# Optimization experiments

Measured on AMD Instinct MI355X. Metric: run time of the kernel, lower is better.

## Reference

```python
import jax, jax.numpy as jnp
import numpy as np

B, L, G, N, K, E = 64, 512, 128, 32, 8, 65536
NTOK, D_TOK, H_DIR, NTL_INP, NHID, NREL = 10000, 64, 64, 32, 16, 16


def _bn(x, gamma, beta, eps=1e-5):
    # training-mode BatchNorm1d over axis 0; x: (n, C)
    mu = x.mean(0)
    var = x.var(0)
    return gamma * (x - mu) / jnp.sqrt(var + eps) + beta


def _lstm(x, w_ih, w_hh, b_ih, b_hh):
    # x: (B, T, D); torch gate order i, f, g, o
    nb = x.shape[0]
    H = w_hh.shape[1]
    def step(carry, xt):
        h, c = carry
        g = xt @ w_ih.T + b_ih + h @ w_hh.T + b_hh
        i, f, gg, o = jnp.split(g, 4, axis=-1)
        c = jax.nn.sigmoid(f) * c + jax.nn.sigmoid(i) * jnp.tanh(gg)
        h = jax.nn.sigmoid(o) * jnp.tanh(c)
        return (h, c), h
    init = (jnp.zeros((nb, H), x.dtype), jnp.zeros((nb, H), x.dtype))
    _, hs = jax.lax.scan(step, init, jnp.swapaxes(x, 0, 1))
    return jnp.swapaxes(hs, 0, 1)


def setup_inputs() -> dict:
    key = jax.random.key(0)
    ks = jax.random.split(key, 24)
    inp = {}
    inp['seq'] = jax.random.randint(ks[0], (B, L), 0, NTOK)
    inp['pos2grp'] = jax.random.randint(ks[1], (B, L), 0, G)
    inp['idx'] = jax.random.randint(ks[2], (B, N, K), 0, L)
    inp['u'] = jax.random.randint(ks[3], (E,), 0, B * N)
    inp['v'] = jax.random.randint(ks[4], (E,), 0, B * N)
    # parameters
    s = 1.0 / np.sqrt(H_DIR)
    inp['tok_emb'] = jax.random.normal(ks[5], (NTOK, D_TOK), jnp.float32)
    for tag, k0 in (('f', 6), ('b', 10)):
        inp[f'w_ih_{tag}'] = s * jax.random.normal(ks[k0], (4 * H_DIR, D_TOK), jnp.float32)
        inp[f'w_hh_{tag}'] = s * jax.random.normal(ks[k0 + 1], (4 * H_DIR, H_DIR), jnp.float32)
        inp[f'b_ih_{tag}'] = s * jax.random.normal(ks[k0 + 2], (4 * H_DIR,), jnp.float32)
        inp[f'b_hh_{tag}'] = s * jax.random.normal(ks[k0 + 3], (4 * H_DIR,), jnp.float32)
    inp['w_src'] = (1.0 / np.sqrt(2 * H_DIR)) * jax.random.normal(ks[14], (NTL_INP, 2 * H_DIR), jnp.float32)
    inp['b_src'] = jnp.zeros((NTL_INP,), jnp.float32)
    inp['w_dst'] = (1.0 / np.sqrt(2 * H_DIR)) * jax.random.normal(ks[15], (NTL_INP, 2 * H_DIR), jnp.float32)
    inp['b_dst'] = jnp.zeros((NTL_INP,), jnp.float32)
    inp['g_src'] = jnp.ones((NTL_INP,), jnp.float32)
    inp['be_src'] = jnp.zeros((NTL_INP,), jnp.float32)
    inp['g_dst'] = jnp.ones((NTL_INP,), jnp.float32)
    inp['be_dst'] = jnp.zeros((NTL_INP,), jnp.float32)
    inp['ntl_w'] = 0.001 * jax.random.normal(ks[16], (NREL, NHID, NTL_INP, NTL_INP), jnp.float32)
    inp['ntl_v'] = 0.001 * jax.random.normal(ks[17], (NREL, NHID, 2 * NTL_INP), jnp.float32)
    inp['ntl_b'] = jnp.zeros((NREL, NHID, 1), jnp.float32)
    inp['ntl_u'] = 0.001 * jax.random.normal(ks[18], (NREL, 1, NHID), jnp.float32)
    inp['ntl_g'] = jnp.ones((NREL * NHID,), jnp.float32)
    inp['ntl_be'] = jnp.zeros((NREL * NHID,), jnp.float32)
    return inp


def reference(seq, pos2grp, idx, u, v, tok_emb,
              w_ih_f, w_hh_f, b_ih_f, b_hh_f,
              w_ih_b, w_hh_b, b_ih_b, b_hh_b,
              w_src, b_src, w_dst, b_dst,
              g_src, be_src, g_dst, be_dst,
              ntl_w, ntl_v, ntl_b, ntl_u, ntl_g, ntl_be):
    # token embed + scatter-sum tokens -> groups
    x_tok = tok_emb[seq]                                   # (B, L, D)
    gid = (pos2grp + jnp.arange(B)[:, None] * G).reshape(-1)
    x_grp = jax.ops.segment_sum(x_tok.reshape(B * L, -1), gid,
                                num_segments=B * G).reshape(B, G, -1)
    # bidirectional LSTM over groups
    hf = _lstm(x_grp, w_ih_f, w_hh_f, b_ih_f, b_hh_f)
    hb = jnp.flip(_lstm(jnp.flip(x_grp, 1), w_ih_b, w_hh_b, b_ih_b, b_hh_b), 1)
    h_grp = jnp.concatenate([hf, hb], -1)                  # (B, G, 2H)
    # hierarchical gather + sum: node <- sum over K token positions' groups
    b_idx = jnp.arange(B)[:, None, None]
    g_idx = pos2grp[b_idx, idx]                            # (B, N, K)
    h = h_grp[b_idx, g_idx].sum(2).reshape(B * N, -1)      # (B*N, 2H)
    # edge endpoint projections + batchnorm
    hs = _bn(h[u] @ w_src.T + b_src, g_src, be_src)        # (E, ninp)
    ht = _bn(h[v] @ w_dst.T + b_dst, g_dst, be_dst)
    # Neural Tensor Layer
    linear = jnp.einsum('rhd,nd->rhn', ntl_v, jnp.concatenate([hs, ht], 1))
    bil = jnp.stack([
        jnp.einsum('nhj,nj->hn', jnp.einsum('ni,hij->nhj', hs, ntl_w[r]), ht)
        for r in range(NREL)], 0)                          # (R, H, E)
    z = bil + linear + ntl_b
    mu = z.mean(-1, keepdims=True)
    var = z.var(-1, keepdims=True)
    zn = ntl_g.reshape(NREL, NHID, 1) * (z - mu) / jnp.sqrt(var + 1e-5) \
         + ntl_be.reshape(NREL, NHID, 1)
    t = jnp.tanh(zn)
    logit = jnp.einsum('rh,rhn->nr', ntl_u[:, 0, :], t)    # (E, R)
    return logit
```

## Files before the change

kernel.cpp:

```cpp
#include <hip/hip_runtime.h>
#include <hip/hip_bf16.h>
#include <hip/hip_fp16.h>
#include <cstdint>

constexpr int B_   = 64;
constexpr int L_   = 512;
constexpr int G_   = 128;
constexpr int E_   = 65536;
constexpr int RH   = 256;
constexpr int M_   = 2048;
constexpr int JA   = 33;
constexpr int COLS = RH * JA;

typedef _Float16 v2h __attribute__((ext_vector_type(2)));

#define DEV static __device__ __forceinline__

DEV float sigm(float x) { return 1.f / (1.f + __expf(-x)); }
DEV float tanh_fast(float x) {
    x = fminf(15.f, fmaxf(-15.f, x));
    float e = __expf(2.f * x);
    return (e - 1.f) / (e + 1.f);
}
DEV int rfl(int x) { return __builtin_amdgcn_readfirstlane(x); }
DEV v2h bch(unsigned int x) { union { unsigned int u; v2h h; } c; c.u = x; return c.h; }

__global__ __launch_bounds__(256) void k_waug(const float* __restrict__ ntlw,
                                              const float* __restrict__ ntlv,
                                              const float* __restrict__ ntlb,
                                              float* __restrict__ waug) {
    int gid = blockIdx.x * 256 + threadIdx.x;
    int i   = gid / COLS;
    int rem = gid - i * COLS;
    int j   = rem >> 8;
    int rh  = rem & 255;
    float val;
    if (i < 32) val = (j < 32) ? ntlw[((size_t)rh * 32 + i) * 32 + j] : ntlv[rh * 64 + i];
    else        val = (j < 32) ? ntlv[rh * 64 + 32 + j] : ntlb[rh];
    waug[gid] = val;
}

__global__ __launch_bounds__(256) void k_eh(const int* __restrict__ seq,
                                            const int* __restrict__ p2g,
                                            const float* __restrict__ emb,
                                            const int* __restrict__ u,
                                            const int* __restrict__ v,
                                            float* __restrict__ xg,
                                            int* __restrict__ cu, int* __restrict__ cv) {
    int blk = blockIdx.x;
    int t   = threadIdx.x;
    if (blk >= 64) {
        int n = (blk - 64) * 256 + t;
        atomicAdd(&cu[u[n]], 1);
        atomicAdd(&cv[v[n]], 1);
        return;
    }
    __shared__ float xgl[G_ * 64];
    for (int i = t; i < G_ * 64; i += 256) xgl[i] = 0.f;
    __syncthreads();
    int b = blk;
    int d = t & 63, part = t >> 6;
#pragma unroll 8
    for (int l = part; l < L_; l += 4) {
        int s = seq[b * L_ + l];
        int g = p2g[b * L_ + l];
        atomicAdd(&xgl[g * 64 + d], emb[s * 64 + d]);
    }
    __syncthreads();
    for (int i = t; i < G_ * 64; i += 256) xg[(size_t)b * G_ * 64 + i] = xgl[i];
}

__global__ __launch_bounds__(256) void k_pre(const float* __restrict__ xg,
                                             const float* __restrict__ wihf,
                                             const float* __restrict__ bihf,
                                             const float* __restrict__ bhhf,
                                             const float* __restrict__ wihb,
                                             const float* __restrict__ bihb,
                                             const float* __restrict__ bhhb,
                                             float* __restrict__ pre,
                                             const int* __restrict__ cu,
                                             int* __restrict__ ustart,
                                             int* __restrict__ ucursor) {
    int blk = blockIdx.x;
    int t   = threadIdx.x;
    if (blk == 512) {
        __shared__ int ps[256];
        int base = t * 8, run = 0;
        int c[8], loc[8];
#pragma unroll
        for (int i = 0; i < 8; i++) c[i] = cu[base + i];
#pragma unroll
        for (int i = 0; i < 8; i++) { loc[i] = run; run += c[i]; }
        ps[t] = run;
        __syncthreads();
        for (int off = 1; off < 256; off <<= 1) {
            int a = (t >= off) ? ps[t - off] : 0;
            __syncthreads();
            ps[t] += a;
            __syncthreads();
        }
        int ex = ps[t] - run;
#pragma unroll
        for (int i = 0; i < 8; i++) { ustart[base + i] = ex + loc[i]; ucursor[base + i] = ex + loc[i]; }
        if (t == 255) ustart[2048] = E_;
        return;
    }
    int dir = blk >> 8;
    const float* wih = dir ? wihb : wihf;
    float bias = dir ? (bihb[t] + bhhb[t]) : (bihf[t] + bhhf[t]);
    int r0 = (blk & 255) * 32;

    float4 wv[16];
#pragma unroll
    for (int c = 0; c < 16; c++) wv[c] = ((const float4*)(wih + t * 64))[c];

#pragma unroll 2
    for (int ml = 0; ml < 32; ml++) {
        const float* xr = xg + (size_t)(r0 + ml) * 64;
        float acc = bias;
#pragma unroll
        for (int c = 0; c < 16; c++) {
            float x0 = xr[4 * c], x1 = xr[4 * c + 1], x2 = xr[4 * c + 2], x3 = xr[4 * c + 3];
            acc += x0 * wv[c].x + x1 * wv[c].y + x2 * wv[c].z + x3 * wv[c].w;
        }
        pre[((size_t)dir * 8192 + r0 + ml) * 256 + t] = acc;
    }
}

template <int HALF>
__global__ __launch_bounds__(256, 1) void k_lstm_h(const float* __restrict__ pre,
                                                   const float* __restrict__ whh_f,
                                                   const float* __restrict__ whh_b,
                                                   float* __restrict__ hgrp,
                                                   float* __restrict__ hstate,
                                                   float* __restrict__ cstate,
                                                   const int* __restrict__ u,
                                                   const int* __restrict__ v,
                                                   int* __restrict__ ucursor,
                                                   int2* __restrict__ eonv) {
    int blk = blockIdx.x;
    int t   = threadIdx.x;
    if (HALF == 0 && blk >= 128) {
        int n = (blk - 128) * 256 + t;
        int pos = atomicAdd(&ucursor[u[n]], 1);
        eonv[pos] = make_int2(n, v[n]);
        return;
    }
    __shared__ __align__(16) float plds[64][256];
    __shared__ __align__(16) float hist[64][64];
    __shared__ float gl[2][256];
    int dir = blk >> 6;
    int b   = blk & 63;
    const float* whh = dir ? whh_b : whh_f;
    const float* src = pre + ((size_t)dir * 8192 + (size_t)b * G_) * 256;
    int e = t & 63;
    int q = t >> 6;

    float4 wv[16];
#pragma unroll
    for (int c = 0; c < 16; c++) wv[c] = ((const float4*)(whh + (size_t)t * 64))[c];

    float h, creg;
    if (HALF == 0) { h = 0.f; creg = 0.f; }
    else           { h = hstate[blk * 64 + e]; creg = cstate[blk * 64 + e]; }

    {
        int base = (dir ^ HALF) ? 64 : 0;
        const float4* s4 = (const float4*)(src + (size_t)base * 256);
        float4* d4 = (float4*)&plds[0][0];
#pragma unroll
        for (int i = 0; i < 16; i++) d4[i * 256 + t] = s4[i * 256 + t];
    }
    __syncthreads();
    for (int kk = 0; kk < 64; kk++) {
        int srow = dir ? (63 - kk) : kk;
        float p = plds[srow][t];
        float a0 = p, a1 = 0.f, a2 = 0.f, a3 = 0.f;
#pragma unroll
        for (int c = 0; c < 16; c++) {
            float f0 = __int_as_float(__builtin_amdgcn_readlane(__float_as_int(h), 4 * c + 0));
            float f1 = __int_as_float(__builtin_amdgcn_readlane(__float_as_int(h), 4 * c + 1));
            float f2 = __int_as_float(__builtin_amdgcn_readlane(__float_as_int(h), 4 * c + 2));
            float f3 = __int_as_float(__builtin_amdgcn_readlane(__float_as_int(h), 4 * c + 3));
            a0 += wv[c].x * f0;
            a1 += wv[c].y * f1;
            a2 += wv[c].z * f2;
            a3 += wv[c].w * f3;
        }
        float g = (a0 + a1) + (a2 + a3);
        gl[kk & 1][t] = (q == 2) ? tanh_fast(g) : sigm(g);
        __syncthreads();
        float ai = gl[kk & 1][e];
        float af = gl[kk & 1][64 + e];
        float ag = gl[kk & 1][128 + e];
        float ao = gl[kk & 1][192 + e];
        creg = af * creg + ai * ag;
        h = ao * tanh_fast(creg);
        if (q == 0) hist[srow][e] = h;
    }
    __syncthreads();
    int sbase = (dir ? (1 - HALF) : HALF) * 64;
#pragma unroll
    for (int i = 0; i < 16; i++) {
        int row = q * 16 + i;
        int s = sbase + row;
        hgrp[((size_t)(b * G_ + s)) * 128 + dir * 64 + e] = hist[row][e];
    }
    if (HALF == 0 && q == 0) {
        hstate[blk * 64 + e] = h;
        cstate[blk * 64 + e] = creg;
    }
}

__global__ __launch_bounds__(256) void k_gp(const int* __restrict__ idx,
                                            const int* __restrict__ p2g,
                                            const float* __restrict__ hgrp,
                                            const int* __restrict__ cu,
                                            const int* __restrict__ cv,
                                            const float* __restrict__ wsrc,
                                            const float* __restrict__ bsrc,
                                            const float* __restrict__ wdst,
                                            const float* __restrict__ bdst,
                                            float* __restrict__ Ps, float* __restrict__ Pd,
                                            float* __restrict__ bn_raw) {
    __shared__ __align__(16) float hsl[8][128];
    __shared__ float red[256];
    int m0 = blockIdx.x * 8;
    int t  = threadIdx.x;
    int d = t & 127, mh = t >> 7;
#pragma unroll
    for (int rep = 0; rep < 4; rep++) {
        int ml = rep * 2 + mh;
        int m  = m0 + ml;
        int b  = m >> 5;
        float acc = 0.f;
#pragma unroll
        for (int k = 0; k < 8; k++) {
            int l = idx[m * 8 + k];
            int g = p2g[b * L_ + l];
            acc += hgrp[((size_t)b * G_ + g) * 128 + d];
        }
        hsl[ml][d] = acc;
    }
    __syncthreads();
    int ml = t >> 5, o = t & 31;
    int m  = m0 + ml;
    const float4* hp = (const float4*)&hsl[ml][0];
    float cw_u = (float)cu[m], cw_v = (float)cv[m];
#pragma unroll 1
    for (int side = 0; side < 2; side++) {
        const float* W = side ? wdst : wsrc;
        float4 wr[32];
#pragma unroll
        for (int c = 0; c < 32; c++) wr[c] = ((const float4*)(W + (size_t)o * 128))[c];
        float acc = side ? bdst[o] : bsrc[o];
#pragma unroll
        for (int c = 0; c < 32; c++) {
            float4 h4 = hp[c];
            acc += h4.x * wr[c].x + h4.y * wr[c].y + h4.z * wr[c].z + h4.w * wr[c].w;
        }
        (side ? Pd : Ps)[(size_t)m * 32 + o] = acc;
        float cw = side ? cw_v : cw_u;
        red[t] = cw * acc;
        __syncthreads();
        if (t < 32) {
            float s = 0.f;
#pragma unroll
            for (int i = 0; i < 8; i++) s += red[i * 32 + t];
            atomicAdd(&bn_raw[side * 64 + t], s);
        }
        __syncthreads();
        red[t] = cw * acc * acc;
        __syncthreads();
        if (t < 32) {
            float s = 0.f;
#pragma unroll
            for (int i = 0; i < 8; i++) s += red[i * 32 + t];
            atomicAdd(&bn_raw[side * 64 + 32 + t], s);
        }
        __syncthreads();
    }
}

__global__ __launch_bounds__(256) void k_prep(const float* __restrict__ Ps,
                                              const float* __restrict__ Pd,
                                              const float* __restrict__ bn_raw,
                                              const float* __restrict__ gs,
                                              const float* __restrict__ bes,
                                              const float* __restrict__ gd,
                                              const float* __restrict__ bed,
                                              float* __restrict__ hsaugT,
                                              v2h* __restrict__ htp) {
    int blk = blockIdx.x;
    int t   = threadIdx.x;
    constexpr float invE = 1.f / (float)E_;
    if (blk < 264) {
        int gid = blk * 256 + t;
        int c = gid >> 11;
        int m = gid & 2047;
        float val = 1.f;
        if (c < 32) {
            float mu  = bn_raw[c] * invE;
            float isd = rsqrtf(bn_raw[32 + c] * invE - mu * mu + 1e-5f);
            val = gs[c] * (Ps[(size_t)m * 32 + c] - mu) * isd + bes[c];
        }
        hsaugT[(size_t)c * 2048 + m] = val;
        return;
    }
    int gid = (blk - 264) * 256 + t;
    int m  = gid >> 4;
    int jp = gid & 15;
    int j0 = 2 * jp, j1 = 2 * jp + 1;
    float mu0  = bn_raw[64 + j0] * invE;
    float isd0 = rsqrtf(bn_raw[96 + j0] * invE - mu0 * mu0 + 1e-5f);
    float mu1  = bn_raw[64 + j1] * invE;
    float isd1 = rsqrtf(bn_raw[96 + j1] * invE - mu1 * mu1 + 1e-5f);
    float h0 = gd[j0] * (Pd[(size_t)m * 32 + j0] - mu0) * isd0 + bed[j0];
    float h1 = gd[j1] * (Pd[(size_t)m * 32 + j1] - mu1) * isd1 + bed[j1];
    v2h p;
    p.x = (_Float16)h0; p.y = (_Float16)h1;
    htp[gid] = p;
}

__global__ __launch_bounds__(256) void k_agemm(const float* __restrict__ hsaugT,
                                               const float* __restrict__ waug,
                                               v2h* __restrict__ Ah,
                                               float* __restrict__ A32) {
    int mt = blockIdx.x;
    int jp = blockIdx.y;
    int t  = threadIdx.x;
    if (jp < 16) {
        float w0[JA], w1[JA];
#pragma unroll
        for (int i = 0; i < JA; i++) {
            w0[i] = waug[(size_t)i * COLS + (2 * jp) * 256 + t];
            w1[i] = waug[(size_t)i * COLS + (2 * jp + 1) * 256 + t];
        }
        float acc0[32], acc1[32];
#pragma unroll
        for (int ml = 0; ml < 32; ml++) { acc0[ml] = 0.f; acc1[ml] = 0.f; }
#pragma unroll 3
        for (int i = 0; i < JA; i++) {
            const float* hr = hsaugT + (size_t)i * 2048 + mt * 32;
#pragma unroll
            for (int ml = 0; ml < 32; ml++) {
                acc0[ml] += hr[ml] * w0[i];
                acc1[ml] += hr[ml] * w1[i];
            }
        }
#pragma unroll
        for (int ml = 0; ml < 32; ml++) {
            v2h p;
            p.x = (_Float16)acc0[ml]; p.y = (_Float16)acc1[ml];
            Ah[(size_t)(mt * 32 + ml) * 4096 + jp * 256 + t] = p;
        }
    } else {
        float w2[JA];
#pragma unroll
        for (int i = 0; i < JA; i++) w2[i] = waug[(size_t)i * COLS + 32 * 256 + t];
        float acc[32];
#pragma unroll
        for (int ml = 0; ml < 32; ml++) acc[ml] = 0.f;
#pragma unroll 3
        for (int i = 0; i < JA; i++) {
            const float* hr = hsaugT + (size_t)i * 2048 + mt * 32;
#pragma unroll
            for (int ml = 0; ml < 32; ml++) acc[ml] += hr[ml] * w2[i];
        }
#pragma unroll
        for (int ml = 0; ml < 32; ml++)
            A32[(size_t)(mt * 32 + ml) * 256 + t] = acc[ml];
    }
}

DEV void load_htp(unsigned int* d, const unsigned int* __restrict__ htp, int vv) {
    const unsigned int* hp = htp + vv * 16;
#pragma unroll
    for (int i = 0; i < 16; i++) d[i] = hp[i];
}
DEV void edge_fd(const unsigned int* av, const unsigned int* ht, float av32,
                 int n, int t, _Float16* __restrict__ zh, float& s1, float& s2) {
    float acc = av32;
#pragma unroll
    for (int jp = 0; jp < 16; jp++)
        acc = __builtin_amdgcn_fdot2(bch(av[jp]), bch(ht[jp]), acc, false);
    zh[(size_t)n * 256 + t] = (_Float16)acc;
    s1 += acc; s2 += acc * acc;
}

__global__ __launch_bounds__(256) void k_z(const unsigned int* __restrict__ Ah,
                                           const float* __restrict__ A32,
                                           const unsigned int* __restrict__ htp,
                                           const int* __restrict__ ustart,
                                           const int2* __restrict__ eonv,
                                           _Float16* __restrict__ zh,
                                           float* __restrict__ zsum,
                                           float* __restrict__ zsq) {
    int t  = threadIdx.x;
    int uu = blockIdx.x;
    float s1 = 0.f, s2 = 0.f;
    unsigned int av[16];
#pragma unroll
    for (int jp = 0; jp < 16; jp++)
        av[jp] = Ah[(size_t)uu * 4096 + jp * 256 + t];
    float av32 = A32[(size_t)uu * 256 + t];
    int e0 = ustart[uu], e1 = ustart[uu + 1];
    if (e0 < e1) {
        int e = e0;
        int2 q0 = eonv[e];
        int n0 = rfl(q0.x), v0 = rfl(q0.y);
        unsigned int ht0[16]; load_htp(ht0, htp, v0);
        int n1 = 0; unsigned int ht1[16];
        while (true) {
            if (e + 1 < e1) {
                int2 q = eonv[e + 1];
                n1 = rfl(q.x); int v1 = rfl(q.y);
                load_htp(ht1, htp, v1);
            }
            edge_fd(av, ht0, av32, n0, t, zh, s1, s2);
            if (++e >= e1) break;
            if (e + 1 < e1) {
                int2 q = eonv[e + 1];
                n0 = rfl(q.x); int v0b = rfl(q.y);
                load_htp(ht0, htp, v0b);
            }
            edge_fd(av, ht1, av32, n1, t, zh, s1, s2);
            if (++e >= e1) break;
        }
    }
    atomicAdd(&zsum[t], s1);
    atomicAdd(&zsq[t], s2);
}

__global__ __launch_bounds__(256) void k_logit(const _Float16* __restrict__ zh,
                                               const float* __restrict__ zsum,
                                               const float* __restrict__ zsq,
                                               const float* __restrict__ ntlu,
                                               const float* __restrict__ ntlg,
                                               const float* __restrict__ ntlbe,
                                               float* __restrict__ out) {
    int t  = threadIdx.x;
    int n0 = blockIdx.x * 16;
    float mu  = zsum[t] / (float)E_;
    float var = zsq[t] / (float)E_ - mu * mu;
    float isd = rsqrtf(var + 1e-5f);
    float g   = ntlg[t],  be  = ntlbe[t];
    float uw  = ntlu[t];
    float zv[16];
#pragma unroll
    for (int nl = 0; nl < 16; nl++)
        zv[nl] = (float)zh[(size_t)(n0 + nl) * 256 + t];
#pragma unroll 1
    for (int nl = 0; nl < 16; nl++) {
        float zn  = g * (zv[nl] - mu) * isd + be;
        float val = uw * tanh_fast(zn);
        val += __shfl_xor(val, 1);
        val += __shfl_xor(val, 2);
        val += __shfl_xor(val, 4);
        val += __shfl_xor(val, 8);
        if ((t & 15) == 0) out[(size_t)(n0 + nl) * 16 + (t >> 4)] = val;
    }
}

extern "C" void kernel_launch(void* const* d_in, const int* in_sizes, int n_in,
                              void* d_out, int out_size, void* d_ws, size_t ws_size,
                              hipStream_t stream) {
    const int*   seq   = (const int*)d_in[0];
    const int*   p2g   = (const int*)d_in[1];
    const int*   idx   = (const int*)d_in[2];
    const int*   u     = (const int*)d_in[3];
    const int*   v     = (const int*)d_in[4];
    const float* emb   = (const float*)d_in[5];
    const float* wihf  = (const float*)d_in[6];
    const float* whhf  = (const float*)d_in[7];
    const float* bihf  = (const float*)d_in[8];
    const float* bhhf  = (const float*)d_in[9];
    const float* wihb  = (const float*)d_in[10];
    const float* whhb  = (const float*)d_in[11];
    const float* bihb  = (const float*)d_in[12];
    const float* bhhb  = (const float*)d_in[13];
    const float* wsrc  = (const float*)d_in[14];
    const float* bsrc  = (const float*)d_in[15];
    const float* wdst  = (const float*)d_in[16];
    const float* bdst  = (const float*)d_in[17];
    const float* gs    = (const float*)d_in[18];
    const float* bes   = (const float*)d_in[19];
    const float* gd    = (const float*)d_in[20];
    const float* bed   = (const float*)d_in[21];
    const float* ntlw  = (const float*)d_in[22];
    const float* ntlv  = (const float*)d_in[23];
    const float* ntlb  = (const float*)d_in[24];
    const float* ntlu  = (const float*)d_in[25];
    const float* ntlg  = (const float*)d_in[26];
    const float* ntlbe = (const float*)d_in[27];
    float* out = (float*)d_out;

    char* ws = (char*)d_ws;
    size_t off = 0;
    auto take = [&](size_t bytes) -> char* {
        char* p = ws + off;
        off = (off + bytes + 255) & ~(size_t)255;
        return p;
    };
    int*   cnt_u  = (int*)  take(2048 * 4);
    int*   cnt_v  = (int*)  take(2048 * 4);
    float* zsum   = (float*)take(256 * 4);
    float* zsq    = (float*)take(256 * 4);
    float* bn_raw = (float*)take(128 * 4);
    size_t zero_bytes = off;
    float* x_grp   = (float*)take((size_t)B_ * G_ * 64 * 4);
    int*   ucursor = (int*)  take(2048 * 4);
    int*   ustart  = (int*)  take(2049 * 4);
    int2*  eonv    = (int2*) take((size_t)E_ * 8);
    float* pre     = (float*)take((size_t)2 * 8192 * 256 * 4);
    float* hgrp    = (float*)take((size_t)B_ * G_ * 128 * 4);
    float* hstate  = (float*)take((size_t)128 * 64 * 4);
    float* cstate  = (float*)take((size_t)128 * 64 * 4);
    float* Psrc    = (float*)take((size_t)M_ * 32 * 4);
    float* Pdst    = (float*)take((size_t)M_ * 32 * 4);
    float* hsaugT  = (float*)take((size_t)36 * 2048 * 4);
    v2h*   htp     = (v2h*)  take((size_t)M_ * 16 * 4);
    float* waug    = (float*)take((size_t)JA * COLS * 4);
    v2h*   Ah      = (v2h*)  take((size_t)M_ * 4096 * 4);
    float* A32     = (float*)take((size_t)M_ * 256 * 4);
    _Float16* zbuf = (_Float16*)take((size_t)E_ * 256 * 2);
    (void)ws_size; (void)in_sizes; (void)n_in; (void)out_size;

    hipMemsetAsync(d_ws, 0, zero_bytes, stream);

    k_waug<<<1089, 256, 0, stream>>>(ntlw, ntlv, ntlb, waug);
    k_eh<<<320, 256, 0, stream>>>(seq, p2g, emb, u, v, x_grp, cnt_u, cnt_v);
    k_pre<<<513, 256, 0, stream>>>(x_grp, wihf, bihf, bhhf, wihb, bihb, bhhb, pre,
                                   cnt_u, ustart, ucursor);
    k_lstm_h<0><<<384, 256, 0, stream>>>(pre, whhf, whhb, hgrp, hstate, cstate,
                                         u, v, ucursor, eonv);
    k_lstm_h<1><<<128, 256, 0, stream>>>(pre, whhf, whhb, hgrp, hstate, cstate,
                                         u, v, ucursor, eonv);
    k_gp<<<M_ / 8, 256, 0, stream>>>(idx, p2g, hgrp, cnt_u, cnt_v,
                                     wsrc, bsrc, wdst, bdst, Psrc, Pdst, bn_raw);
    k_prep<<<392, 256, 0, stream>>>(Psrc, Pdst, bn_raw, gs, bes, gd, bed, hsaugT, htp);
    k_agemm<<<dim3(64, 17), 256, 0, stream>>>(hsaugT, waug, Ah, A32);
    k_z<<<M_, 256, 0, stream>>>((const unsigned int*)Ah, A32, (const unsigned int*)htp,
                                ustart, eonv, zbuf, zsum, zsq);
    k_logit<<<E_ / 16, 256, 0, stream>>>(zbuf, zsum, zsq, ntlu, ntlg, ntlbe, out);
}
```

Before: 421.8 us.

## Fuse waug build into k_eh and batch-pipeline edge loads in k_z

The separate weight-augmentation kernel is folded into k_eh as extra blocks, which removes one launch, and the source indexing is remapped so reads are coalesced along the source. k_z now stages each row's edge list in LDS in chunks of 128 and double-buffers groups of four edges' ht vectors, loaded as uint4. The fdot2 chain is split into four independent accumulators to shorten the dependency chain. In exchange, register pressure grows from the 2x4x4 uint4 buffers, and the per-chunk syncthreads add some overhead.

New measurement: 417.9 us. Within noise of the previous version (-0.9%).

```diff
diff --git a/kernel.cpp b/kernel.cpp
--- a/kernel.cpp
+++ b/kernel.cpp
@@ -24,20 +24,8 @@
 }
 DEV int rfl(int x) { return __builtin_amdgcn_readfirstlane(x); }
 DEV v2h bch(unsigned int x) { union { unsigned int u; v2h h; } c; c.u = x; return c.h; }
-
-__global__ __launch_bounds__(256) void k_waug(const float* __restrict__ ntlw,
-                                              const float* __restrict__ ntlv,
-                                              const float* __restrict__ ntlb,
-                                              float* __restrict__ waug) {
-    int gid = blockIdx.x * 256 + threadIdx.x;
-    int i   = gid / COLS;
-    int rem = gid - i * COLS;
-    int j   = rem >> 8;
-    int rh  = rem & 255;
-    float val;
-    if (i < 32) val = (j < 32) ? ntlw[((size_t)rh * 32 + i) * 32 + j] : ntlv[rh * 64 + i];
-    else        val = (j < 32) ? ntlv[rh * 64 + 32 + j] : ntlb[rh];
-    waug[gid] = val;
+DEV float fd2(unsigned int a, unsigned int b, float c) {
+    return __builtin_amdgcn_fdot2(bch(a), bch(b), c, false);
 }
 
 __global__ __launch_bounds__(256) void k_eh(const int* __restrict__ seq,
@@ -45,10 +33,26 @@
                                             const float* __restrict__ emb,
                                             const int* __restrict__ u,
                                             const int* __restrict__ v,
+                                            const float* __restrict__ ntlw,
+                                            const float* __restrict__ ntlv,
+                                            const float* __restrict__ ntlb,
                                             float* __restrict__ xg,
-                                            int* __restrict__ cu, int* __restrict__ cv) {
+                                            int* __restrict__ cu, int* __restrict__ cv,
+                                            float* __restrict__ waug) {
     int blk = blockIdx.x;
     int t   = threadIdx.x;
+    if (blk >= 320) {
+        int gid = (blk - 320) * 256 + t;
+        int i   = gid / COLS;
+        int rem = gid - i * COLS;
+        int rh  = rem / JA;
+        int j   = rem - rh * JA;
+        float val;
+        if (i < 32) val = (j < 32) ? ntlw[((size_t)rh * 32 + i) * 32 + j] : ntlv[rh * 64 + i];
+        else        val = (j < 32) ? ntlv[rh * 64 + 32 + j] : ntlb[rh];
+        waug[(size_t)i * COLS + j * 256 + rh] = val;
+        return;
+    }
     if (blk >= 64) {
         int n = (blk - 64) * 256 + t;
         atomicAdd(&cu[u[n]], 1);
@@ -373,29 +377,15 @@
     }
 }
 
-DEV void load_htp(unsigned int* d, const unsigned int* __restrict__ htp, int vv) {
-    const unsigned int* hp = htp + vv * 16;
-#pragma unroll
-    for (int i = 0; i < 16; i++) d[i] = hp[i];
-}
-DEV void edge_fd(const unsigned int* av, const unsigned int* ht, float av32,
-                 int n, int t, _Float16* __restrict__ zh, float& s1, float& s2) {
-    float acc = av32;
-#pragma unroll
-    for (int jp = 0; jp < 16; jp++)
-        acc = __builtin_amdgcn_fdot2(bch(av[jp]), bch(ht[jp]), acc, false);
-    zh[(size_t)n * 256 + t] = (_Float16)acc;
-    s1 += acc; s2 += acc * acc;
-}
-
 __global__ __launch_bounds__(256) void k_z(const unsigned int* __restrict__ Ah,
                                            const float* __restrict__ A32,
-                                           const unsigned int* __restrict__ htp,
+                                           const uint4* __restrict__ htp4,
                                            const int* __restrict__ ustart,
                                            const int2* __restrict__ eonv,
                                            _Float16* __restrict__ zh,
                                            float* __restrict__ zsum,
                                            float* __restrict__ zsq) {
+    __shared__ int ldsnn[128], ldsvv[128];
     int t  = threadIdx.x;
     int uu = blockIdx.x;
     float s1 = 0.f, s2 = 0.f;
@@ -405,27 +395,69 @@
         av[jp] = Ah[(size_t)uu * 4096 + jp * 256 + t];
     float av32 = A32[(size_t)uu * 256 + t];
     int e0 = ustart[uu], e1 = ustart[uu + 1];
-    if (e0 < e1) {
-        int e = e0;
-        int2 q0 = eonv[e];
-        int n0 = rfl(q0.x), v0 = rfl(q0.y);
-        unsigned int ht0[16]; load_htp(ht0, htp, v0);
-        int n1 = 0; unsigned int ht1[16];
-        while (true) {
-            if (e + 1 < e1) {
-                int2 q = eonv[e + 1];
-                n1 = rfl(q.x); int v1 = rfl(q.y);
-                load_htp(ht1, htp, v1);
+
+    uint4 bufA[4][4], bufB[4][4];
+
+    for (int base = e0; base < e1; base += 128) {
+        int cnt = min(128, e1 - base);
+        __syncthreads();
+        for (int i = t; i < cnt; i += 256) {
+            int2 q = eonv[base + i];
+            ldsnn[i] = q.x; ldsvv[i] = q.y;
+        }
+        __syncthreads();
+        int ngrp = (cnt + 3) >> 2;
+
+        auto loadgrp = [&](uint4 (&buf)[4][4], int g) {
+#pragma unroll
+            for (int ee = 0; ee < 4; ee++) {
+                int gi = g * 4 + ee;
+                int ix = min(gi, cnt - 1);
+                int vvv = rfl(ldsvv[ix]);
+                const uint4* hrow = htp4 + (size_t)vvv * 4;
+                buf[ee][0] = hrow[0]; buf[ee][1] = hrow[1];
+                buf[ee][2] = hrow[2]; buf[ee][3] = hrow[3];
             }
-            edge_fd(av, ht0, av32, n0, t, zh, s1, s2);
-            if (++e >= e1) break;
-            if (e + 1 < e1) {
-                int2 q = eonv[e + 1];
-                n0 = rfl(q.x); int v0b = rfl(q.y);
-                load_htp(ht0, htp, v0b);
+        };
+        auto compgrp = [&](uint4 (&buf)[4][4], int g) {
+#pragma unroll
+            for (int ee = 0; ee < 4; ee++) {
+                int gi = g * 4 + ee;
+                if (gi < cnt) {
+                    uint4 b0 = buf[ee][0], b1 = buf[ee][1], b2 = buf[ee][2], b3 = buf[ee][3];
+                    float c0 = fd2(av[0],  b0.x, av32);
+                    float c1 = fd2(av[1],  b0.y, 0.f);
+                    float c2 = fd2(av[2],  b0.z, 0.f);
+                    float c3 = fd2(av[3],  b0.w, 0.f);
+                    c0 = fd2(av[4],  b1.x, c0);
+                    c1 = fd2(av[5],  b1.y, c1);
+                    c2 = fd2(av[6],  b1.z, c2);
+                    c3 = fd2(av[7],  b1.w, c3);
+                    c0 = fd2(av[8],  b2.x, c0);
+                    c1 = fd2(av[9],  b2.y, c1);
+                    c2 = fd2(av[10], b2.z, c2);
+                    c3 = fd2(av[11], b2.w, c3);
+                    c0 = fd2(av[12], b3.x, c0);
+                    c1 = fd2(av[13], b3.y, c1);
+                    c2 = fd2(av[14], b3.z, c2);
+                    c3 = fd2(av[15], b3.w, c3);
+                    float acc = (c0 + c1) + (c2 + c3);
+                    int nnv = rfl(ldsnn[gi]);
+                    zh[(size_t)nnv * 256 + t] = (_Float16)acc;
+                    s1 += acc; s2 += acc * acc;
+                }
             }
-            edge_fd(av, ht1, av32, n1, t, zh, s1, s2);
-            if (++e >= e1) break;
+        };
+
+        if (ngrp > 0) {
+            loadgrp(bufA, 0);
+            for (int g = 0; g < ngrp; g += 2) {
+                if (g + 1 < ngrp) loadgrp(bufB, g + 1);
+                compgrp(bufA, g);
+                if (g + 1 >= ngrp) break;
+                if (g + 2 < ngrp) loadgrp(bufA, g + 2);
+                compgrp(bufB, g + 1);
+            }
         }
     }
     atomicAdd(&zsum[t], s1);
@@ -528,8 +560,8 @@
 
     hipMemsetAsync(d_ws, 0, zero_bytes, stream);
 
-    k_waug<<<1089, 256, 0, stream>>>(ntlw, ntlv, ntlb, waug);
-    k_eh<<<320, 256, 0, stream>>>(seq, p2g, emb, u, v, x_grp, cnt_u, cnt_v);
+    k_eh<<<320 + 1089, 256, 0, stream>>>(seq, p2g, emb, u, v, ntlw, ntlv, ntlb,
+                                         x_grp, cnt_u, cnt_v, waug);
     k_pre<<<513, 256, 0, stream>>>(x_grp, wihf, bihf, bhhf, wihb, bihb, bhhb, pre,
                                    cnt_u, ustart, ucursor);
     k_lstm_h<0><<<384, 256, 0, stream>>>(pre, whhf, whhb, hgrp, hstate, cstate,
@@ -540,7 +572,7 @@
                                      wsrc, bsrc, wdst, bdst, Psrc, Pdst, bn_raw);
     k_prep<<<392, 256, 0, stream>>>(Psrc, Pdst, bn_raw, gs, bes, gd, bed, hsaugT, htp);
     k_agemm<<<dim3(64, 17), 256, 0, stream>>>(hsaugT, waug, Ah, A32);
-    k_z<<<M_, 256, 0, stream>>>((const unsigned int*)Ah, A32, (const unsigned int*)htp,
+    k_z<<<M_, 256, 0, stream>>>((const unsigned int*)Ah, A32, (const uint4*)htp,
                                 ustart, eonv, zbuf, zsum, zsq);
     k_logit<<<E_ / 16, 256, 0, stream>>>(zbuf, zsum, zsq, ntlu, ntlg, ntlbe, out);
 }
```

## Compute per-edge bilinear scores with MFMA tiles and fold waug build into k_eh

Applied to the files above, without the earlier changes.

Rewrites k_z so each wavefront owns one source node and processes 16 edges at a time with a 16x16x32 f16 MFMA. This replaces the per-thread fdot2 loop that handled one edge per iteration. Row statistics are reduced with cross-lane shuffles before the atomics. The waug weight-reshaping kernel is merged into k_eh as extra blocks to save a launch, and its indexing is changed so the write pattern differs. Edge tails are padded and masked, and zh stores are now scattered 16-wide per row, which may coalesce less well.

After: 418.7 us. No clear change (-0.7%).

```diff
diff --git a/kernel.cpp b/kernel.cpp
--- a/kernel.cpp
+++ b/kernel.cpp
@@ -13,6 +13,9 @@
 constexpr int COLS = RH * JA;
 
 typedef _Float16 v2h __attribute__((ext_vector_type(2)));
+typedef _Float16 v8h __attribute__((ext_vector_type(8)));
+typedef float    v4f __attribute__((ext_vector_type(4)));
+typedef union { uint4 u4; v8h h8; } cvt8;
 
 #define DEV static __device__ __forceinline__
 
@@ -22,33 +25,32 @@
     float e = __expf(2.f * x);
     return (e - 1.f) / (e + 1.f);
 }
-DEV int rfl(int x) { return __builtin_amdgcn_readfirstlane(x); }
-DEV v2h bch(unsigned int x) { union { unsigned int u; v2h h; } c; c.u = x; return c.h; }
-
-__global__ __launch_bounds__(256) void k_waug(const float* __restrict__ ntlw,
-                                              const float* __restrict__ ntlv,
-                                              const float* __restrict__ ntlb,
-                                              float* __restrict__ waug) {
-    int gid = blockIdx.x * 256 + threadIdx.x;
-    int i   = gid / COLS;
-    int rem = gid - i * COLS;
-    int j   = rem >> 8;
-    int rh  = rem & 255;
-    float val;
-    if (i < 32) val = (j < 32) ? ntlw[((size_t)rh * 32 + i) * 32 + j] : ntlv[rh * 64 + i];
-    else        val = (j < 32) ? ntlv[rh * 64 + 32 + j] : ntlb[rh];
-    waug[gid] = val;
-}
 
 __global__ __launch_bounds__(256) void k_eh(const int* __restrict__ seq,
                                             const int* __restrict__ p2g,
                                             const float* __restrict__ emb,
                                             const int* __restrict__ u,
                                             const int* __restrict__ v,
+                                            const float* __restrict__ ntlw,
+                                            const float* __restrict__ ntlv,
+                                            const float* __restrict__ ntlb,
                                             float* __restrict__ xg,
-                                            int* __restrict__ cu, int* __restrict__ cv) {
+                                            int* __restrict__ cu, int* __restrict__ cv,
+                                            float* __restrict__ waug) {
     int blk = blockIdx.x;
     int t   = threadIdx.x;
+    if (blk >= 320) {
+        int gid = (blk - 320) * 256 + t;
+        int i   = gid / COLS;
+        int rem = gid - i * COLS;
+        int rh  = rem / JA;
+        int j   = rem - rh * JA;
+        float val;
+        if (i < 32) val = (j < 32) ? ntlw[((size_t)rh * 32 + i) * 32 + j] : ntlv[rh * 64 + i];
+        else        val = (j < 32) ? ntlv[rh * 64 + 32 + j] : ntlb[rh];
+        waug[(size_t)i * COLS + j * 256 + rh] = val;
+        return;
+    }
     if (blk >= 64) {
         int n = (blk - 64) * 256 + t;
         atomicAdd(&cu[u[n]], 1);
@@ -373,63 +375,71 @@
     }
 }
 
-DEV void load_htp(unsigned int* d, const unsigned int* __restrict__ htp, int vv) {
-    const unsigned int* hp = htp + vv * 16;
-#pragma unroll
-    for (int i = 0; i < 16; i++) d[i] = hp[i];
-}
-DEV void edge_fd(const unsigned int* av, const unsigned int* ht, float av32,
-                 int n, int t, _Float16* __restrict__ zh, float& s1, float& s2) {
-    float acc = av32;
-#pragma unroll
-    for (int jp = 0; jp < 16; jp++)
-        acc = __builtin_amdgcn_fdot2(bch(av[jp]), bch(ht[jp]), acc, false);
-    zh[(size_t)n * 256 + t] = (_Float16)acc;
-    s1 += acc; s2 += acc * acc;
-}
-
 __global__ __launch_bounds__(256) void k_z(const unsigned int* __restrict__ Ah,
                                            const float* __restrict__ A32,
-                                           const unsigned int* __restrict__ htp,
+                                           const uint4* __restrict__ htp4,
                                            const int* __restrict__ ustart,
                                            const int2* __restrict__ eonv,
                                            _Float16* __restrict__ zh,
                                            float* __restrict__ zsum,
                                            float* __restrict__ zsq) {
-    int t  = threadIdx.x;
-    int uu = blockIdx.x;
-    float s1 = 0.f, s2 = 0.f;
-    unsigned int av[16];
-#pragma unroll
-    for (int jp = 0; jp < 16; jp++)
-        av[jp] = Ah[(size_t)uu * 4096 + jp * 256 + t];
-    float av32 = A32[(size_t)uu * 256 + t];
+    int t    = threadIdx.x;
+    int lane = t & 63;
+    int uu   = blockIdx.x * 4 + (t >> 6);
+    int l15  = lane & 15, quad = lane >> 4;
+
+    uint4 bf[16];
+#pragma unroll
+    for (int nt = 0; nt < 16; nt++) {
+        const unsigned int* bp = Ah + (size_t)uu * 4096 + (quad * 4) * 256 + nt * 16 + l15;
+        bf[nt].x = bp[0]; bf[nt].y = bp[256]; bf[nt].z = bp[512]; bf[nt].w = bp[768];
+    }
+    float a32[16];
+#pragma unroll
+    for (int nt = 0; nt < 16; nt++) a32[nt] = A32[(size_t)uu * 256 + nt * 16 + l15];
+
+    float s1[16], s2[16];
+#pragma unroll
+    for (int nt = 0; nt < 16; nt++) { s1[nt] = 0.f; s2[nt] = 0.f; }
+
     int e0 = ustart[uu], e1 = ustart[uu + 1];
-    if (e0 < e1) {
-        int e = e0;
-        int2 q0 = eonv[e];
-        int n0 = rfl(q0.x), v0 = rfl(q0.y);
-        unsigned int ht0[16]; load_htp(ht0, htp, v0);
-        int n1 = 0; unsigned int ht1[16];
-        while (true) {
-            if (e + 1 < e1) {
-                int2 q = eonv[e + 1];
-                n1 = rfl(q.x); int v1 = rfl(q.y);
-                load_htp(ht1, htp, v1);
+    for (int base = e0; base < e1; base += 16) {
+        int ei = min(base + l15, e1 - 1);
+        int2 q = eonv[ei];
+        uint4 afu = htp4[(size_t)q.y * 4 + quad];
+        cvt8 ac; ac.u4 = afu;
+        int nrow[4], valid[4];
+#pragma unroll
+        for (int r = 0; r < 4; r++) {
+            int er = quad * 4 + r;
+            nrow[r]  = __builtin_amdgcn_ds_bpermute(er << 2, q.x);
+            valid[r] = (base + er) < e1;
+        }
+#pragma unroll
+        for (int nt = 0; nt < 16; nt++) {
+            cvt8 bc; bc.u4 = bf[nt];
+            v4f acc = { a32[nt], a32[nt], a32[nt], a32[nt] };
+            acc = __builtin_amdgcn_mfma_f32_16x16x32_f16(ac.h8, bc.h8, acc, 0, 0, 0);
+#pragma unroll
+            for (int r = 0; r < 4; r++) {
+                if (valid[r]) {
+                    float z = acc[r];
+                    zh[(size_t)nrow[r] * 256 + nt * 16 + l15] = (_Float16)z;
+                    s1[nt] += z; s2[nt] += z * z;
+                }
             }
-            edge_fd(av, ht0, av32, n0, t, zh, s1, s2);
-            if (++e >= e1) break;
-            if (e + 1 < e1) {
-                int2 q = eonv[e + 1];
-                n0 = rfl(q.x); int v0b = rfl(q.y);
-                load_htp(ht0, htp, v0b);
-            }
-            edge_fd(av, ht1, av32, n1, t, zh, s1, s2);
-            if (++e >= e1) break;
-        }
-    }
-    atomicAdd(&zsum[t], s1);
-    atomicAdd(&zsq[t], s2);
+        }
+    }
+#pragma unroll
+    for (int nt = 0; nt < 16; nt++) {
+        float a = s1[nt], b = s2[nt];
+        a += __shfl_xor(a, 16); a += __shfl_xor(a, 32);
+        b += __shfl_xor(b, 16); b += __shfl_xor(b, 32);
+        if (quad == 0) {
+            atomicAdd(&zsum[nt * 16 + l15], a);
+            atomicAdd(&zsq[nt * 16 + l15], b);
+        }
+    }
 }
 
 __global__ __launch_bounds__(256) void k_logit(const _Float16* __restrict__ zh,
@@ -528,8 +538,8 @@
 
     hipMemsetAsync(d_ws, 0, zero_bytes, stream);
 
-    k_waug<<<1089, 256, 0, stream>>>(ntlw, ntlv, ntlb, waug);
-    k_eh<<<320, 256, 0, stream>>>(seq, p2g, emb, u, v, x_grp, cnt_u, cnt_v);
+    k_eh<<<320 + 1089, 256, 0, stream>>>(seq, p2g, emb, u, v, ntlw, ntlv, ntlb,
+                                         x_grp, cnt_u, cnt_v, waug);
     k_pre<<<513, 256, 0, stream>>>(x_grp, wihf, bihf, bhhf, wihb, bihb, bhhb, pre,
                                    cnt_u, ustart, ucursor);
     k_lstm_h<0><<<384, 256, 0, stream>>>(pre, whhf, whhb, hgrp, hstate, cstate,
@@ -540,7 +550,7 @@
                                      wsrc, bsrc, wdst, bdst, Psrc, Pdst, bn_raw);
     k_prep<<<392, 256, 0, stream>>>(Psrc, Pdst, bn_raw, gs, bes, gd, bed, hsaugT, htp);
     k_agemm<<<dim3(64, 17), 256, 0, stream>>>(hsaugT, waug, Ah, A32);
-    k_z<<<M_, 256, 0, stream>>>((const unsigned int*)Ah, A32, (const unsigned int*)htp,
-                                ustart, eonv, zbuf, zsum, zsq);
+    k_z<<<512, 256, 0, stream>>>((const unsigned int*)Ah, A32, (const uint4*)htp,
+                                 ustart, eonv, zbuf, zsum, zsq);
     k_logit<<<E_ / 16, 256, 0, stream>>>(zbuf, zsum, zsq, ntlu, ntlg, ntlbe, out);
 }
```
